# Performance work log

Measured on AMD Instinct MI355X. Metric: run time of the kernel, lower is better.

## Reference

```python
import jax, jax.numpy as jnp
import numpy as np

B, N, L = 16, 128, 512            # batch, scan length, per-step feature (= configs.seq_len)
D, S, K, R, H = 1024, 16, 4, 64, 2048  # d_model, d_state, ker_size, dt_rank, hidden_dimention


def _mamba_params(key, scale=0.02):
    ks = jax.random.split(key, 6)
    return dict(
        in_w=jax.random.normal(ks[0], (2 * D, L)) * scale,
        conv_w=jax.random.normal(ks[1], (D, K)) * scale,
        conv_b=jnp.zeros((D,)),
        xproj_w=jax.random.normal(ks[2], (R + 2 * S, D)) * scale,
        dt_w=jax.random.normal(ks[3], (D, R)) * scale,
        dt_b=jax.random.normal(ks[4], (D,)) * scale,
        A_log=jnp.tile(jnp.log(jnp.arange(1, S + 1, dtype=jnp.float32)), (D, 1)),
        Dp=jnp.ones((D,)),
        out_w=jax.random.normal(ks[5], (L, D)) * scale,
    )


def setup_inputs():
    key = jax.random.key(0)
    kx, kf, kr, k1, k2 = jax.random.split(key, 5)
    inp = {"x": jax.random.normal(kx, (B, N, L), dtype=jnp.float32)}
    for pre, k in (("f_", kf), ("r_", kr)):
        for n, v in _mamba_params(k).items():
            inp[pre + n] = v
    inp["pu_w"] = jax.random.normal(k1, (H, L)) * 0.02
    inp["pu_b"] = jnp.zeros((H,))
    inp["pl_w"] = jax.random.normal(k2, (L, H)) * 0.02
    inp["pl_b"] = jnp.zeros((L,))
    inp["ln_g"] = jnp.ones((L,))
    inp["ln_b"] = jnp.zeros((L,))
    return inp


def _ln(x, g, b, eps=1e-5):
    m = x.mean(-1, keepdims=True)
    v = ((x - m) ** 2).mean(-1, keepdims=True)
    return (x - m) * jax.lax.rsqrt(v + eps) * g + b


def _dw_causal_conv(x, w, b):
    # x: [B,N,D]; depthwise causal conv along N with kernel [D,K]
    xt = jnp.pad(x.transpose(0, 2, 1), ((0, 0), (0, 0), (K - 1, 0)))  # [B,D,N+K-1]
    y = jax.lax.conv_general_dilated(xt, w[:, None, :], (1,), 'VALID',
                                     dimension_numbers=('NCH', 'OIH', 'NCH'),
                                     feature_group_count=D)
    return (y + b[None, :, None]).transpose(0, 2, 1)


def _mamba(x, in_w, conv_w, conv_b, xproj_w, dt_w, dt_b, A_log, Dp, out_w):
    # standard Mamba block (in_proj -> depthwise conv -> silu -> selective scan -> gate -> out_proj)
    xi, res = jnp.split(x @ in_w.T, 2, axis=-1)             # [B,N,D] each
    xc = jax.nn.silu(_dw_causal_conv(xi, conv_w, conv_b))   # [B,N,D]
    dbc = xc @ xproj_w.T                                    # [B,N,R+2S]
    dt, Bm, Cm = dbc[..., :R], dbc[..., R:R + S], dbc[..., R + S:]
    delta = jax.nn.softplus(dt @ dt_w.T + dt_b)             # [B,N,D]
    A = -jnp.exp(A_log)                                     # [D,S]
    dA = jnp.exp(delta[..., None] * A)                      # [B,N,D,S]
    dBx = delta[..., None] * Bm[:, :, None, :] * xc[..., None]

    def step(h, t):
        dA_t, dBx_t, C_t = t
        h = dA_t * h + dBx_t                                # [B,D,S]
        return h, jnp.einsum('bds,bs->bd', h, C_t)

    _, ys = jax.lax.scan(step, jnp.zeros((x.shape[0], D, S), x.dtype),
                         (dA.transpose(1, 0, 2, 3), dBx.transpose(1, 0, 2, 3), Cm.transpose(1, 0, 2)))
    y = ys.transpose(1, 0, 2) + xc * Dp                     # [B,N,D]
    y = y * jax.nn.silu(res)
    return y @ out_w.T                                      # [B,N,L]


def reference(x, f_in_w, f_conv_w, f_conv_b, f_xproj_w, f_dt_w, f_dt_b, f_A_log, f_Dp, f_out_w,
              r_in_w, r_conv_w, r_conv_b, r_xproj_w, r_dt_w, r_dt_b, r_A_log, r_Dp, r_out_w,
              pu_w, pu_b, pl_w, pl_b, ln_g, ln_b):
    y1 = _mamba(x, f_in_w, f_conv_w, f_conv_b, f_xproj_w, f_dt_w, f_dt_b, f_A_log, f_Dp, f_out_w)
    y2 = _mamba(x[:, ::-1, :], r_in_w, r_conv_w, r_conv_b, r_xproj_w, r_dt_w, r_dt_b, r_A_log, r_Dp, r_out_w)
    y3 = _ln(x + y1 + y2[:, ::-1, :], ln_g, ln_b)
    yp = jax.nn.relu(y3 @ pu_w.T + pu_b)
    yp = yp @ pl_w.T + pl_b
    return _ln(yp + y3, ln_g, ln_b)
```

## Files before the change

kernel.cpp:

```cpp
#include <hip/hip_runtime.h>
#include <hip/hip_bf16.h>
#include <cstdint>

typedef __hip_bfloat16 bf16;

constexpr int Bb = 16, Nn = 128, Ll = 512, Dd = 1024, Ss = 16, Rr = 64, Hh = 2048;
constexpr int Mm = Bb * Nn;

using bf16x8 = __attribute__((ext_vector_type(8))) __bf16;
using bf16x4 = __attribute__((ext_vector_type(4))) __bf16;
using f32x4  = __attribute__((ext_vector_type(4))) float;

__device__ __forceinline__ float to_f(float x) { return x; }
__device__ __forceinline__ float to_f(bf16 x) { return __bfloat162float(x); }
__device__ __forceinline__ void store_t(float* p, float v) { *p = v; }
__device__ __forceinline__ void store_t(bf16* p, float v) { *p = __float2bfloat16(v); }
__device__ __forceinline__ __bf16 cvt1(float x) {
  bf16 h = __float2bfloat16(x);
  return *reinterpret_cast<__bf16*>(&h);
}
__device__ __forceinline__ float bfraw_to_f(__bf16 x) {
  bf16 h = *reinterpret_cast<bf16*>(&x);
  return __bfloat162float(h);
}
__device__ __forceinline__ bf16x8 load8(const bf16* p) { return *(const bf16x8*)p; }
__device__ __forceinline__ bf16x8 load8(const float* p) {
  float4 a = *(const float4*)p;
  float4 b = *(const float4*)(p + 4);
  bf16x8 r;
  r[0] = cvt1(a.x); r[1] = cvt1(a.y); r[2] = cvt1(a.z); r[3] = cvt1(a.w);
  r[4] = cvt1(b.x); r[5] = cvt1(b.y); r[6] = cvt1(b.z); r[7] = cvt1(b.w);
  return r;
}
__device__ __forceinline__ bf16x8 load8rt(const void* p, size_t idx, int isbf) {
  if (isbf) return load8((const bf16*)p + idx);
  return load8((const float*)p + idx);
}
__device__ __forceinline__ float ldf(const void* p, int i, int isbf) {
  if (isbf) return __bfloat162float(((const bf16*)p)[i]);
  return ((const float*)p)[i];
}

enum { EPI_STORE = 0, EPI_BIAS_RELU = 1, EPI_ADD = 3, EPI_BIAS = 4, EPI_BIAS_SOFTPLUS = 5,
       EPI_ATOMIC = 6 };

__global__ void sniff_kernel(const unsigned short* __restrict__ xs, int* __restrict__ flags) {
  const int tid = threadIdx.x;
  int cnt = 0;
  for (int j = 0; j < 64; ++j) {
    int i = tid + j * 256;
    unsigned short u = xs[(size_t)i * 64];
    bf16 h = *reinterpret_cast<bf16*>(&u);
    float v = __bfloat162float(h);
    float a = fabsf(v);
    if (v == 0.f || (a > 0.0009765625f && a < 16.f)) ++cnt;
  }
  __shared__ int sc[256];
  sc[tid] = cnt;
  __syncthreads();
  for (int o = 128; o > 0; o >>= 1) {
    if (tid < o) sc[tid] += sc[tid + o];
    __syncthreads();
  }
  if (tid == 0) flags[0] = (sc[0] > 8192) ? 1 : 0;
}

constexpr int LDT2 = 72;
template <typename TC, int EPI>
__global__ __launch_bounds__(256) void gemm_rt(
    const int* __restrict__ flagp,
    const void* __restrict__ A, int lda, int abf,
    const void* __restrict__ Bw, const void* __restrict__ Bw2, int ldb,
    int bmode, int bsplit,
    TC* __restrict__ C, int ldc,
    const void* __restrict__ bias, const void* __restrict__ bias2,
    int N, int Kchunk, int zk, size_t a_doff, size_t c_doff) {
  const int isbf = *flagp;
  const int ab = (abf == 2) ? isbf : abf;
  __shared__ __align__(16) __bf16 As[64 * LDT2];
  __shared__ __align__(16) __bf16 Bs[64 * LDT2];
  const int tid = threadIdx.x;
  const int wave = tid >> 6, lane = tid & 63;
  const int quad = lane >> 4, l16 = lane & 15;
  const int wm = wave & 1, wn = wave >> 1;
  int bx = blockIdx.x, by = blockIdx.y;
  const int gx = gridDim.x, gy = gridDim.y;
  if ((gx & 7) == 0) {
    int id = bx + gx * by;
    int xcd = id & 7, sl = id >> 3;
    by = sl % gy;
    bx = (sl / gy) * 8 + xcd;
  }
  int zsl = blockIdx.z;
  const void* Ap = A;
  const void* Bp0 = Bw;
  const void* biasp = bias;
  if (bmode == 3) {
    const int dir = zsl / zk;
    zsl = zsl % zk;
    if (dir) {
      Ap = (const char*)A + a_doff * (size_t)(ab ? 2 : 4);
      C += c_doff;
      Bp0 = Bw2;
      biasp = bias2;
    }
  }
  const int m0 = by * 64, n0 = bx * 64;
  const int kb = zsl * Kchunk;
  const int srow = tid >> 3;
  const int scol = (tid & 7) * 8;
  f32x4 acc[2][2] = {};
  for (int k0 = kb; k0 < kb + Kchunk; k0 += 64) {
#pragma unroll
    for (int h = 0; h < 2; ++h) {
      int r = srow + h * 32;
      *(bf16x8*)(&As[r * LDT2 + scol]) =
          load8rt(Ap, (size_t)(m0 + r) * lda + k0 + scol, ab);
      int rb = n0 + r;
      rb = rb < N ? rb : N - 1;
      const void* bp = Bp0;
      size_t bi;
      const int kk = k0 + scol;
      if (bmode == 1 && rb >= bsplit) {
        bp = Bw2; bi = (size_t)(rb - bsplit) * ldb + kk;
      } else if (bmode == 2 && kk >= bsplit) {
        bp = Bw2; bi = (size_t)rb * ldb + (kk - bsplit);
      } else {
        bi = (size_t)rb * ldb + kk;
      }
      *(bf16x8*)(&Bs[r * LDT2 + scol]) = load8rt(bp, bi, isbf);
    }
    __syncthreads();
#pragma unroll
    for (int kk2 = 0; kk2 < 2; ++kk2) {
      bf16x8 af[2], bfr[2];
#pragma unroll
      for (int i = 0; i < 2; ++i)
        af[i] = *(const bf16x8*)(&As[(wm * 32 + i * 16 + l16) * LDT2 + kk2 * 32 + quad * 8]);
#pragma unroll
      for (int j = 0; j < 2; ++j)
        bfr[j] = *(const bf16x8*)(&Bs[(wn * 32 + j * 16 + l16) * LDT2 + kk2 * 32 + quad * 8]);
#pragma unroll
      for (int i = 0; i < 2; ++i)
#pragma unroll
        for (int j = 0; j < 2; ++j)
          acc[i][j] = __builtin_amdgcn_mfma_f32_16x16x32_bf16(af[i], bfr[j], acc[i][j], 0, 0, 0);
    }
    __syncthreads();
  }
#pragma unroll
  for (int i = 0; i < 2; ++i) {
#pragma unroll
    for (int j = 0; j < 2; ++j) {
      const int col = n0 + wn * 32 + j * 16 + l16;
      if (col >= N) continue;
      float bv = 0.f;
      if (EPI == EPI_BIAS_RELU || EPI == EPI_BIAS || EPI == EPI_BIAS_SOFTPLUS)
        bv = ldf(biasp, col, isbf);
#pragma unroll
      for (int r = 0; r < 4; ++r) {
        const int row = m0 + wm * 32 + i * 16 + quad * 4 + r;
        size_t idx = (size_t)row * ldc + col;
        float v = acc[i][j][r];
        if (EPI == EPI_STORE) store_t(&C[idx], v);
        else if (EPI == EPI_BIAS_RELU) { v += bv; store_t(&C[idx], v > 0.f ? v : 0.f); }
        else if (EPI == EPI_BIAS) store_t(&C[idx], v + bv);
        else if (EPI == EPI_BIAS_SOFTPLUS) {
          v += bv;
          store_t(&C[idx], (v > 20.f) ? v : log1pf(__expf(v)));
        } else if (EPI == EPI_ATOMIC) {
          atomicAdd((float*)&C[idx], v);
        }
      }
    }
  }
}

__global__ __launch_bounds__(256) void zero_kernel(float4* __restrict__ p, int n4) {
  int i = blockIdx.x * 256 + threadIdx.x;
  if (i < n4) p[i] = float4{0.f, 0.f, 0.f, 0.f};
}

__global__ __launch_bounds__(256) void init_zbuf_rt(const int* __restrict__ flagp,
                                                    const void* __restrict__ x,
                                                    float* __restrict__ ZB) {
  const int isbf = *flagp;
  int i = blockIdx.x * 256 + threadIdx.x;
  float4 o;
  if (isbf) {
    ushort4 u = ((const ushort4*)x)[i];
    bf16 h0 = *reinterpret_cast<bf16*>(&u.x), h1 = *reinterpret_cast<bf16*>(&u.y);
    bf16 h2 = *reinterpret_cast<bf16*>(&u.z), h3 = *reinterpret_cast<bf16*>(&u.w);
    o = float4{__bfloat162float(h0), __bfloat162float(h1),
               __bfloat162float(h2), __bfloat162float(h3)};
  } else {
    o = ((const float4*)x)[i];
  }
  ((float4*)ZB)[i] = o;
}

__global__ __launch_bounds__(256) void conv_silu_rt(
    const int* __restrict__ flagp, const float* __restrict__ X2,
    const void* __restrict__ fcw, const void* __restrict__ fcb,
    const void* __restrict__ rcw, const void* __restrict__ rcb,
    float* __restrict__ XC) {
  const int isbf = *flagp;
  const int dir = blockIdx.y >> 2;
  const int d = (blockIdx.y & 3) * 256 + threadIdx.x;
  const int m = blockIdx.x;
  const int t = m & (Nn - 1);
  const void* cw = dir ? rcw : fcw;
  const void* cb = dir ? rcb : fcb;
  float w0 = ldf(cw, d * 4 + 0, isbf), w1 = ldf(cw, d * 4 + 1, isbf);
  float w2 = ldf(cw, d * 4 + 2, isbf), w3 = ldf(cw, d * 4 + 3, isbf);
  float a = ldf(cb, d, isbf);
  const size_t base = (size_t)m * 4096 + (size_t)dir * 2048 + d;
  if (dir == 0) {
    if (t >= 3) a += w0 * X2[base - 3 * 4096];
    if (t >= 2) a += w1 * X2[base - 2 * 4096];
    if (t >= 1) a += w2 * X2[base - 1 * 4096];
    a += w3 * X2[base];
  } else {
    if (t + 3 < Nn) a += w0 * X2[base + 3 * 4096];
    if (t + 2 < Nn) a += w1 * X2[base + 2 * 4096];
    if (t + 1 < Nn) a += w2 * X2[base + 1 * 4096];
    a += w3 * X2[base];
  }
  XC[(size_t)m * 2048 + (size_t)dir * 1024 + d] = a / (1.f + __expf(-a));
}

__global__ __launch_bounds__(256) void scan_gate_rt(
    const int* __restrict__ flagp,
    const float* __restrict__ DBC0, float* __restrict__ XC, const float* __restrict__ X2,
    const bf16* __restrict__ DELTA0,
    const void* __restrict__ fAlog, const void* __restrict__ fDp,
    const void* __restrict__ rAlog, const void* __restrict__ rDp) {
  const int isbf = *flagp;
  const int dir = blockIdx.z;
  const float* DBC = DBC0 + (size_t)dir * Mm * 96;
  const bf16* DELTA = DELTA0 + (size_t)dir * Mm * 1024;
  const void* A_log = dir ? rAlog : fAlog;
  const void* Dp = dir ? rDp : fDp;
  __shared__ __align__(16) __bf16 sBC[Nn * 32];
  __shared__ __align__(16) __bf16 sD[Nn * 16];
  __shared__ __align__(16) __bf16 sX[Nn * 16];
  __shared__ __align__(16) __bf16 sR[Nn * 16];
  __shared__ float sSdv[Nn * 16];
  __shared__ float sHend[4 * 16 * 16];
  __shared__ float sSdvEnd[4 * 16];
  const int b = blockIdx.x;
  const int d0 = blockIdx.y * 16;
  const int tid = threadIdx.x;
  const size_t rowbase = (size_t)b * Nn;
  const size_t xc_col = (size_t)dir * 1024;
#pragma unroll
  for (int k = 0; k < 16; ++k) {
    int idx = tid + k * 256;
    int t = idx >> 5, c = idx & 31;
    sBC[idx] = cvt1(DBC[(rowbase + t) * 96 + 64 + c]);
  }
  {
    int t = tid >> 1, h = tid & 1;
    *(uint4*)&sD[t * 16 + h * 8] = *(const uint4*)(DELTA + (rowbase + t) * 1024 + d0 + h * 8);
  }
#pragma unroll
  for (int k = 0; k < 2; ++k) {
    int j = tid + k * 256;
    int t = j >> 2, qq = j & 3;
    float4 vx = *(const float4*)(XC + (rowbase + t) * 2048 + xc_col + d0 + qq * 4);
    bf16x4 px = {cvt1(vx.x), cvt1(vx.y), cvt1(vx.z), cvt1(vx.w)};
    *(bf16x4*)&sX[t * 16 + qq * 4] = px;
    float4 vr = *(const float4*)(X2 + (rowbase + t) * 4096 + (size_t)dir * 2048 + 1024 + d0 + qq * 4);
    bf16x4 pr = {cvt1(vr.x), cvt1(vr.y), cvt1(vr.z), cvt1(vr.w)};
    *(bf16x4*)&sR[t * 16 + qq * 4] = pr;
  }
  __syncthreads();
  const int q = tid >> 6;
  const int lane = tid & 63;
  const int dl = lane & 15, sg = lane >> 4;
  const int d = d0 + dl;
  float A_[4];
#pragma unroll
  for (int j = 0; j < 4; ++j) A_[j] = -__expf(ldf(A_log, d * Ss + sg * 4 + j, isbf));
  float h0 = 0.f, h1 = 0.f, h2 = 0.f, h3 = 0.f, Sdv = 0.f;
  for (int j = 0; j < 32; ++j) {
    const int p = q * 32 + j;
    const int t = dir ? (Nn - 1 - p) : p;
    const float dv = bfraw_to_f(sD[t * 16 + dl]);
    const float xv = bfraw_to_f(sX[t * 16 + dl]);
    Sdv += dv;
    bf16x4 Bmv = *(const bf16x4*)&sBC[t * 32 + sg * 4];
    bf16x4 Cmv = *(const bf16x4*)&sBC[t * 32 + 16 + sg * 4];
    const float dx = dv * xv;
    h0 = __expf(dv * A_[0]) * h0 + dx * bfraw_to_f(Bmv[0]);
    h1 = __expf(dv * A_[1]) * h1 + dx * bfraw_to_f(Bmv[1]);
    h2 = __expf(dv * A_[2]) * h2 + dx * bfraw_to_f(Bmv[2]);
    h3 = __expf(dv * A_[3]) * h3 + dx * bfraw_to_f(Bmv[3]);
    float acc = h0 * bfraw_to_f(Cmv[0]) + h1 * bfraw_to_f(Cmv[1]) +
                h2 * bfraw_to_f(Cmv[2]) + h3 * bfraw_to_f(Cmv[3]);
    acc += __shfl_xor(acc, 16, 64);
    acc += __shfl_xor(acc, 32, 64);
    if (sg == 0) {
      sSdv[t * 16 + dl] = Sdv;
      XC[(rowbase + t) * 2048 + xc_col + d] = acc;
    }
  }
  sHend[q * 256 + (sg * 4 + 0) * 16 + dl] = h0;
  sHend[q * 256 + (sg * 4 + 1) * 16 + dl] = h1;
  sHend[q * 256 + (sg * 4 + 2) * 16 + dl] = h2;
  sHend[q * 256 + (sg * 4 + 3) * 16 + dl] = h3;
  if (sg == 0) sSdvEnd[q * 16 + dl] = Sdv;
  __syncthreads();
  if (q == 0) {
    float r0 = 0.f, r1 = 0.f, r2 = 0.f, r3 = 0.f;
    for (int qq = 0; qq < 4; ++qq) {
      const float se = sSdvEnd[qq * 16 + dl];
      const float e0 = __expf(A_[0] * se), e1 = __expf(A_[1] * se);
      const float e2 = __expf(A_[2] * se), e3 = __expf(A_[3] * se);
      const int base = qq * 256 + sg * 4 * 16 + dl;
      float t0 = sHend[base + 0 * 16], t1 = sHend[base + 1 * 16];
      float t2 = sHend[base + 2 * 16], t3 = sHend[base + 3 * 16];
      sHend[base + 0 * 16] = r0; sHend[base + 1 * 16] = r1;
      sHend[base + 2 * 16] = r2; sHend[base + 3 * 16] = r3;
      r0 = e0 * r0 + t0; r1 = e1 * r1 + t1;
      r2 = e2 * r2 + t2; r3 = e3 * r3 + t3;
    }
  }
  __syncthreads();
  {
    const int dl2 = lane & 15, trow = lane >> 4;
    const int d2 = d0 + dl2;
    float A2[16];
#pragma unroll
    for (int s = 0; s < 16; ++s) A2[s] = -__expf(ldf(A_log, d2 * Ss + s, isbf));
    const float dp2 = ldf(Dp, d2, isbf);
    float hin[16];
#pragma unroll
    for (int s = 0; s < 16; ++s) hin[s] = sHend[q * 256 + s * 16 + dl2];
    for (int rep = 0; rep < 8; ++rep) {
      const int p = q * 32 + trow + rep * 4;
      const int t = dir ? (Nn - 1 - p) : p;
      const float Sv = sSdv[t * 16 + dl2];
      float corr = 0.f;
#pragma unroll
      for (int s = 0; s < 16; ++s)
        corr += bfraw_to_f(sBC[t * 32 + 16 + s]) * __expf(A2[s] * Sv) * hin[s];
      const size_t gidx = (rowbase + t) * 2048 + xc_col + d2;
      const float y = XC[gidx] + corr;
      const float xv = bfraw_to_f(sX[t * 16 + dl2]);
      const float res = bfraw_to_f(sR[t * 16 + dl2]);
      const float g = res / (1.f + __expf(-res));
      XC[gidx] = (y + xv * dp2) * g;
    }
  }
}

template <int MODE>
__global__ __launch_bounds__(256) void ln_rt(const int* __restrict__ flagp,
                                             const float* __restrict__ Z,
                                             const float* __restrict__ Zadd,
                                             const void* __restrict__ g,
                                             const void* __restrict__ bb,
                                             const void* __restrict__ pb,
                                             void* __restrict__ outp) {
  const int isbf = *flagp;
  const int row = blockIdx.x;
  const int tid = threadIdx.x;
  const int c0 = tid * 2;
  const float2* z = (const float2*)(Z + (size_t)row * Ll);
  float2 v = z[tid];
  if (MODE == 1) {
    const float2* za = (const float2*)(Zadd + (size_t)row * Ll);
    float2 a = za[tid];
    v.x += a.x + ldf(pb, c0, isbf);
    v.y += a.y + ldf(pb, c0 + 1, isbf);
  }
  float s = v.x + v.y, q = v.x * v.x + v.y * v.y;
#pragma unroll
  for (int o = 32; o > 0; o >>= 1) {
    s += __shfl_xor(s, o, 64);
    q += __shfl_xor(q, o, 64);
  }
  __shared__ float ss[4], qq[4];
  const int wv = tid >> 6, ln = tid & 63;
  if (ln == 0) { ss[wv] = s; qq[wv] = q; }
  __syncthreads();
  s = ss[0] + ss[1] + ss[2] + ss[3];
  q = qq[0] + qq[1] + qq[2] + qq[3];
  const float mean = s * (1.f / Ll);
  const float var = q * (1.f / Ll) - mean * mean;
  const float rs = rsqrtf(var + 1e-5f);
  const float o0 = (v.x - mean) * rs * ldf(g, c0, isbf) + ldf(bb, c0, isbf);
  const float o1 = (v.y - mean) * rs * ldf(g, c0 + 1, isbf) + ldf(bb, c0 + 1, isbf);
  if (MODE == 0) {
    float* out = (float*)outp;
    out[(size_t)row * Ll + c0] = o0;
    out[(size_t)row * Ll + c0 + 1] = o1;
  } else {
    if (isbf) {
      bf16* out = (bf16*)outp;
      out[(size_t)row * Ll + c0] = __float2bfloat16(o0);
      out[(size_t)row * Ll + c0 + 1] = __float2bfloat16(o1);
    } else {
      float* out = (float*)outp;
      out[(size_t)row * Ll + c0] = o0;
      out[(size_t)row * Ll + c0 + 1] = o1;
    }
  }
}

extern "C" void kernel_launch(void* const* d_in, const int* in_sizes, int n_in, void* d_out,
                              int out_size, void* d_ws, size_t ws_size, hipStream_t stream) {
  char* ws = (char*)d_ws;
  int* flags = (int*)ws;
  float* X2 = (float*)(ws + 256);
  float* XC = X2 + (size_t)Mm * 4096;
  float* DBC = XC + (size_t)Mm * 2048;
  float* Z2 = DBC + (size_t)2 * Mm * 96;
  float* ZB = Z2 + (size_t)Mm * 512;
  float* Y3 = ZB + (size_t)Mm * 512;
  bf16* DELTA = (bf16*)(Y3 + (size_t)Mm * 512);
  bf16* H1 = (bf16*)X2;
  size_t needed = 256 + sizeof(float) * ((size_t)Mm * 4096 + (size_t)Mm * 2048 +
                                         (size_t)2 * Mm * 96 + (size_t)3 * Mm * 512 +
                                         (size_t)Mm * 1024);
  if (ws_size < needed) return;

  const void* x = d_in[0];
  const dim3 blk(256);

  sniff_kernel<<<dim3(1), blk, 0, stream>>>((const unsigned short*)x, flags);
  init_zbuf_rt<<<dim3(Mm * Ll / 4 / 256), blk, 0, stream>>>(flags, x, ZB);
  zero_kernel<<<dim3((2 * Mm * 96 + Mm * 512) / 4 / 256), blk, 0, stream>>>(
      (float4*)DBC, (2 * Mm * 96 + Mm * 512) / 4);
  gemm_rt<float, EPI_STORE><<<dim3(64, 32), blk, 0, stream>>>(
      flags, x, Ll, 2, d_in[1], d_in[10], Ll, 1, 2048,
      X2, 4096, nullptr, nullptr, 4096, Ll, 1, 0, 0);
  conv_silu_rt<<<dim3(Mm, 8), blk, 0, stream>>>(flags, X2, d_in[2], d_in[3],
                                                d_in[11], d_in[12], XC);
  gemm_rt<float, EPI_ATOMIC><<<dim3(2, 32, 8), blk, 0, stream>>>(
      flags, XC, 2048, 0, d_in[4], d_in[13], Dd, 3, 0,
      DBC, 96, nullptr, nullptr, 96, 256, 4, 1024, (size_t)Mm * 96);
  gemm_rt<bf16, EPI_BIAS_SOFTPLUS><<<dim3(16, 32, 2), blk, 0, stream>>>(
      flags, DBC, 96, 0, d_in[5], d_in[14], Rr, 3, 0,
      DELTA, 1024, d_in[6], d_in[15], 1024, Rr, 1, (size_t)Mm * 96, (size_t)Mm * 1024);
  scan_gate_rt<<<dim3(Bb, Dd / 16, 2), blk, 0, stream>>>(
      flags, DBC, XC, X2, DELTA, d_in[7], d_in[8], d_in[16], d_in[17]);
  gemm_rt<float, EPI_ATOMIC><<<dim3(8, 32, 4), blk, 0, stream>>>(
      flags, XC, 2048, 0, d_in[9], d_in[18], Dd, 2, 1024,
      ZB, Ll, nullptr, nullptr, Ll, 512, 1, 0, 0);
  ln_rt<0><<<dim3(Mm), blk, 0, stream>>>(flags, ZB, nullptr, d_in[23], d_in[24], nullptr, (void*)Y3);
  gemm_rt<bf16, EPI_BIAS_RELU><<<dim3(32, 32), blk, 0, stream>>>(
      flags, Y3, Ll, 0, d_in[19], nullptr, Ll, 0, 0,
      H1, Hh, d_in[20], nullptr, Hh, Ll, 1, 0, 0);
  gemm_rt<float, EPI_ATOMIC><<<dim3(8, 32, 2), blk, 0, stream>>>(
      flags, H1, Hh, 1, d_in[21], nullptr, Hh, 0, 0,
      Z2, Ll, nullptr, nullptr, Ll, 1024, 1, 0, 0);
  ln_rt<1><<<dim3(Mm), blk, 0, stream>>>(flags, Z2, Y3, d_in[23], d_in[24], d_in[22], d_out);

  (void)in_sizes; (void)n_in; (void)out_size;
}
```

Baseline: 373.4 us.

## Add 128x128-tile GEMM for large projections and recompute scan outputs in second pass

Adds a gemm128 kernel with 128x128 output tiles, 4x4 MFMA fragments per wave and XCD-aware block remapping, and uses it for the in_proj, out_proj and both MLP GEMMs to raise operand reuse per LDS load. The selective-scan kernel no longer writes partial outputs and cumulative delta sums in its first chunk pass. Instead it reruns each chunk's recurrence from the exchanged carry-in states, producing outputs directly and dropping the 16-term exp correction pass and the sSdv buffer. The small-GEMM kernel loses its split-B addressing path. Larger tiles mean fewer blocks and more register pressure, and the scan now does the recurrence twice per chunk.

```diff
diff --git a/kernel.cpp b/kernel.cpp
--- a/kernel.cpp
+++ b/kernel.cpp
@@ -66,6 +66,7 @@
 }
 
 constexpr int LDT2 = 72;
+
 template <typename TC, int EPI>
 __global__ __launch_bounds__(256) void gemm_rt(
     const int* __restrict__ flagp,
@@ -118,17 +119,8 @@
           load8rt(Ap, (size_t)(m0 + r) * lda + k0 + scol, ab);
       int rb = n0 + r;
       rb = rb < N ? rb : N - 1;
-      const void* bp = Bp0;
-      size_t bi;
-      const int kk = k0 + scol;
-      if (bmode == 1 && rb >= bsplit) {
-        bp = Bw2; bi = (size_t)(rb - bsplit) * ldb + kk;
-      } else if (bmode == 2 && kk >= bsplit) {
-        bp = Bw2; bi = (size_t)rb * ldb + (kk - bsplit);
-      } else {
-        bi = (size_t)rb * ldb + kk;
-      }
-      *(bf16x8*)(&Bs[r * LDT2 + scol]) = load8rt(bp, bi, isbf);
+      size_t bi = (size_t)rb * ldb + k0 + scol;
+      *(bf16x8*)(&Bs[r * LDT2 + scol]) = load8rt(Bp0, bi, isbf);
     }
     __syncthreads();
 #pragma unroll
@@ -171,6 +163,93 @@
         } else if (EPI == EPI_ATOMIC) {
           atomicAdd((float*)&C[idx], v);
         }
+      }
+    }
+  }
+}
+
+template <typename TC, int EPI>
+__global__ __launch_bounds__(256) void gemm128(
+    const int* __restrict__ flagp,
+    const void* __restrict__ A, int lda, int abf,
+    const void* __restrict__ Bw, const void* __restrict__ Bw2, int ldb,
+    int bmode, int bsplit,
+    TC* __restrict__ C, int ldc,
+    const void* __restrict__ bias,
+    int N, int Kchunk) {
+  const int isbf = *flagp;
+  const int ab = (abf == 2) ? isbf : abf;
+  __shared__ __align__(16) __bf16 As[128 * LDT2];
+  __shared__ __align__(16) __bf16 Bs[128 * LDT2];
+  const int tid = threadIdx.x;
+  const int wave = tid >> 6, lane = tid & 63;
+  const int quad = lane >> 4, l16 = lane & 15;
+  const int wm = wave & 1, wn = wave >> 1;
+  int bx = blockIdx.x, by = blockIdx.y;
+  const int gx = gridDim.x, gy = gridDim.y;
+  if ((gx & 7) == 0) {
+    int id = bx + gx * by;
+    int xcd = id & 7, sl = id >> 3;
+    by = sl % gy;
+    bx = (sl / gy) * 8 + xcd;
+  }
+  const int m0 = by * 128, n0 = bx * 128;
+  const int kb = blockIdx.z * Kchunk;
+  const int srow = tid >> 3;
+  const int scol = (tid & 7) * 8;
+  f32x4 acc[4][4] = {};
+  for (int k0 = kb; k0 < kb + Kchunk; k0 += 64) {
+#pragma unroll
+    for (int h = 0; h < 4; ++h) {
+      int r = srow + h * 32;
+      *(bf16x8*)(&As[r * LDT2 + scol]) =
+          load8rt(A, (size_t)(m0 + r) * lda + k0 + scol, ab);
+      const int rb = n0 + r;
+      const int kk = k0 + scol;
+      const void* bp = Bw;
+      size_t bi;
+      if (bmode == 1 && rb >= bsplit) {
+        bp = Bw2; bi = (size_t)(rb - bsplit) * ldb + kk;
+      } else if (bmode == 2 && kk >= bsplit) {
+        bp = Bw2; bi = (size_t)rb * ldb + (kk - bsplit);
+      } else {
+        bi = (size_t)rb * ldb + kk;
+      }
+      *(bf16x8*)(&Bs[r * LDT2 + scol]) = load8rt(bp, bi, isbf);
+    }
+    __syncthreads();
+#pragma unroll
+    for (int kk2 = 0; kk2 < 2; ++kk2) {
+      bf16x8 af[4], bfr[4];
+#pragma unroll
+      for (int i = 0; i < 4; ++i)
+        af[i] = *(const bf16x8*)(&As[(wm * 64 + i * 16 + l16) * LDT2 + kk2 * 32 + quad * 8]);
+#pragma unroll
+      for (int j = 0; j < 4; ++j)
+        bfr[j] = *(const bf16x8*)(&Bs[(wn * 64 + j * 16 + l16) * LDT2 + kk2 * 32 + quad * 8]);
+#pragma unroll
+      for (int i = 0; i < 4; ++i)
+#pragma unroll
+        for (int j = 0; j < 4; ++j)
+          acc[i][j] = __builtin_amdgcn_mfma_f32_16x16x32_bf16(af[i], bfr[j], acc[i][j], 0, 0, 0);
+    }
+    __syncthreads();
+  }
+#pragma unroll
+  for (int i = 0; i < 4; ++i) {
+#pragma unroll
+    for (int j = 0; j < 4; ++j) {
+      const int col = n0 + wn * 64 + j * 16 + l16;
+      float bv = 0.f;
+      if (EPI == EPI_BIAS_RELU) bv = ldf(bias, col, isbf);
+#pragma unroll
+      for (int r = 0; r < 4; ++r) {
+        const int row = m0 + wm * 64 + i * 16 + quad * 4 + r;
+        size_t idx = (size_t)row * ldc + col;
+        float v = acc[i][j][r];
+        if (EPI == EPI_STORE) store_t(&C[idx], v);
+        else if (EPI == EPI_BIAS_RELU) { v += bv; store_t(&C[idx], v > 0.f ? v : 0.f); }
+        else if (EPI == EPI_ATOMIC) atomicAdd((float*)&C[idx], v);
       }
     }
   }
@@ -229,7 +308,7 @@
   XC[(size_t)m * 2048 + (size_t)dir * 1024 + d] = a / (1.f + __expf(-a));
 }
 
-__global__ __launch_bounds__(256) void scan_gate_rt(
+__global__ __launch_bounds__(256) void scan_gate2(
     const int* __restrict__ flagp,
     const float* __restrict__ DBC0, float* __restrict__ XC, const float* __restrict__ X2,
     const bf16* __restrict__ DELTA0,
@@ -245,7 +324,6 @@
   __shared__ __align__(16) __bf16 sD[Nn * 16];
   __shared__ __align__(16) __bf16 sX[Nn * 16];
   __shared__ __align__(16) __bf16 sR[Nn * 16];
-  __shared__ float sSdv[Nn * 16];
   __shared__ float sHend[4 * 16 * 16];
   __shared__ float sSdvEnd[4 * 16];
   const int b = blockIdx.x;
@@ -290,20 +368,11 @@
     const float xv = bfraw_to_f(sX[t * 16 + dl]);
     Sdv += dv;
     bf16x4 Bmv = *(const bf16x4*)&sBC[t * 32 + sg * 4];
-    bf16x4 Cmv = *(const bf16x4*)&sBC[t * 32 + 16 + sg * 4];
     const float dx = dv * xv;
     h0 = __expf(dv * A_[0]) * h0 + dx * bfraw_to_f(Bmv[0]);
     h1 = __expf(dv * A_[1]) * h1 + dx * bfraw_to_f(Bmv[1]);
     h2 = __expf(dv * A_[2]) * h2 + dx * bfraw_to_f(Bmv[2]);
     h3 = __expf(dv * A_[3]) * h3 + dx * bfraw_to_f(Bmv[3]);
-    float acc = h0 * bfraw_to_f(Cmv[0]) + h1 * bfraw_to_f(Cmv[1]) +
-                h2 * bfraw_to_f(Cmv[2]) + h3 * bfraw_to_f(Cmv[3]);
-    acc += __shfl_xor(acc, 16, 64);
-    acc += __shfl_xor(acc, 32, 64);
-    if (sg == 0) {
-      sSdv[t * 16 + dl] = Sdv;
-      XC[(rowbase + t) * 2048 + xc_col + d] = acc;
-    }
   }
   sHend[q * 256 + (sg * 4 + 0) * 16 + dl] = h0;
   sHend[q * 256 + (sg * 4 + 1) * 16 + dl] = h1;
@@ -327,30 +396,31 @@
     }
   }
   __syncthreads();
-  {
-    const int dl2 = lane & 15, trow = lane >> 4;
-    const int d2 = d0 + dl2;
-    float A2[16];
-#pragma unroll
-    for (int s = 0; s < 16; ++s) A2[s] = -__expf(ldf(A_log, d2 * Ss + s, isbf));
-    const float dp2 = ldf(Dp, d2, isbf);
-    float hin[16];
-#pragma unroll
-    for (int s = 0; s < 16; ++s) hin[s] = sHend[q * 256 + s * 16 + dl2];
-    for (int rep = 0; rep < 8; ++rep) {
-      const int p = q * 32 + trow + rep * 4;
-      const int t = dir ? (Nn - 1 - p) : p;
-      const float Sv = sSdv[t * 16 + dl2];
-      float corr = 0.f;
-#pragma unroll
-      for (int s = 0; s < 16; ++s)
-        corr += bfraw_to_f(sBC[t * 32 + 16 + s]) * __expf(A2[s] * Sv) * hin[s];
-      const size_t gidx = (rowbase + t) * 2048 + xc_col + d2;
-      const float y = XC[gidx] + corr;
-      const float xv = bfraw_to_f(sX[t * 16 + dl2]);
-      const float res = bfraw_to_f(sR[t * 16 + dl2]);
+  h0 = sHend[q * 256 + (sg * 4 + 0) * 16 + dl];
+  h1 = sHend[q * 256 + (sg * 4 + 1) * 16 + dl];
+  h2 = sHend[q * 256 + (sg * 4 + 2) * 16 + dl];
+  h3 = sHend[q * 256 + (sg * 4 + 3) * 16 + dl];
+  const float dp = ldf(Dp, d, isbf);
+  for (int j = 0; j < 32; ++j) {
+    const int p = q * 32 + j;
+    const int t = dir ? (Nn - 1 - p) : p;
+    const float dv = bfraw_to_f(sD[t * 16 + dl]);
+    const float xv = bfraw_to_f(sX[t * 16 + dl]);
+    bf16x4 Bmv = *(const bf16x4*)&sBC[t * 32 + sg * 4];
+    bf16x4 Cmv = *(const bf16x4*)&sBC[t * 32 + 16 + sg * 4];
+    const float dx = dv * xv;
+    h0 = __expf(dv * A_[0]) * h0 + dx * bfraw_to_f(Bmv[0]);
+    h1 = __expf(dv * A_[1]) * h1 + dx * bfraw_to_f(Bmv[1]);
+    h2 = __expf(dv * A_[2]) * h2 + dx * bfraw_to_f(Bmv[2]);
+    h3 = __expf(dv * A_[3]) * h3 + dx * bfraw_to_f(Bmv[3]);
+    float acc = h0 * bfraw_to_f(Cmv[0]) + h1 * bfraw_to_f(Cmv[1]) +
+                h2 * bfraw_to_f(Cmv[2]) + h3 * bfraw_to_f(Cmv[3]);
+    acc += __shfl_xor(acc, 16, 64);
+    acc += __shfl_xor(acc, 32, 64);
+    if (sg == 0) {
+      const float res = bfraw_to_f(sR[t * 16 + dl]);
       const float g = res / (1.f + __expf(-res));
-      XC[gidx] = (y + xv * dp2) * g;
+      XC[(rowbase + t) * 2048 + xc_col + d] = (acc + xv * dp) * g;
     }
   }
 }
@@ -433,9 +503,9 @@
   init_zbuf_rt<<<dim3(Mm * Ll / 4 / 256), blk, 0, stream>>>(flags, x, ZB);
   zero_kernel<<<dim3((2 * Mm * 96 + Mm * 512) / 4 / 256), blk, 0, stream>>>(
       (float4*)DBC, (2 * Mm * 96 + Mm * 512) / 4);
-  gemm_rt<float, EPI_STORE><<<dim3(64, 32), blk, 0, stream>>>(
+  gemm128<float, EPI_STORE><<<dim3(32, 16), blk, 0, stream>>>(
       flags, x, Ll, 2, d_in[1], d_in[10], Ll, 1, 2048,
-      X2, 4096, nullptr, nullptr, 4096, Ll, 1, 0, 0);
+      X2, 4096, nullptr, 4096, Ll);
   conv_silu_rt<<<dim3(Mm, 8), blk, 0, stream>>>(flags, X2, d_in[2], d_in[3],
                                                 d_in[11], d_in[12], XC);
   gemm_rt<float, EPI_ATOMIC><<<dim3(2, 32, 8), blk, 0, stream>>>(
@@ -444,18 +514,18 @@
   gemm_rt<bf16, EPI_BIAS_SOFTPLUS><<<dim3(16, 32, 2), blk, 0, stream>>>(
       flags, DBC, 96, 0, d_in[5], d_in[14], Rr, 3, 0,
       DELTA, 1024, d_in[6], d_in[15], 1024, Rr, 1, (size_t)Mm * 96, (size_t)Mm * 1024);
-  scan_gate_rt<<<dim3(Bb, Dd / 16, 2), blk, 0, stream>>>(
+  scan_gate2<<<dim3(Bb, Dd / 16, 2), blk, 0, stream>>>(
       flags, DBC, XC, X2, DELTA, d_in[7], d_in[8], d_in[16], d_in[17]);
-  gemm_rt<float, EPI_ATOMIC><<<dim3(8, 32, 4), blk, 0, stream>>>(
+  gemm128<float, EPI_ATOMIC><<<dim3(4, 16, 4), blk, 0, stream>>>(
       flags, XC, 2048, 0, d_in[9], d_in[18], Dd, 2, 1024,
-      ZB, Ll, nullptr, nullptr, Ll, 512, 1, 0, 0);
+      ZB, Ll, nullptr, Ll, 512);
   ln_rt<0><<<dim3(Mm), blk, 0, stream>>>(flags, ZB, nullptr, d_in[23], d_in[24], nullptr, (void*)Y3);
-  gemm_rt<bf16, EPI_BIAS_RELU><<<dim3(32, 32), blk, 0, stream>>>(
+  gemm128<bf16, EPI_BIAS_RELU><<<dim3(16, 16), blk, 0, stream>>>(
       flags, Y3, Ll, 0, d_in[19], nullptr, Ll, 0, 0,
-      H1, Hh, d_in[20], nullptr, Hh, Ll, 1, 0, 0);
-  gemm_rt<float, EPI_ATOMIC><<<dim3(8, 32, 2), blk, 0, stream>>>(
+      H1, Hh, d_in[20], Hh, Ll);
+  gemm128<float, EPI_ATOMIC><<<dim3(4, 16, 4), blk, 0, stream>>>(
       flags, H1, Hh, 1, d_in[21], nullptr, Hh, 0, 0,
-      Z2, Ll, nullptr, nullptr, Ll, 1024, 1, 0, 0);
+      Z2, Ll, nullptr, Ll, 512);
   ln_rt<1><<<dim3(Mm), blk, 0, stream>>>(flags, Z2, Y3, d_in[23], d_in[24], d_in[22], d_out);
 
   (void)in_sizes; (void)n_in; (void)out_size;
```

Result: slower. 414.8 us (+11.1%).

## Store Mamba intermediates in bf16 and recompute chunked scan instead of correction pass

Applied to the files above, without the earlier changes.

The in-projection output and the conv/silu activations move from fp32 to bf16 buffers, roughly halving traffic for the conv, x-projection, scan and out-projection stages. The scan kernel no longer writes partial outputs and then fixes them with a 16-term exponential correction. It now runs a first pass to get chunk-end states, combines them, and reruns the recurrence from the correct starting state, caching delta and x in registers. This removes global read-modify-write and shared prefix-sum storage at the cost of doing the recurrence twice, higher register pressure, and bf16 rounding of the intermediates.

```diff
diff --git a/kernel.cpp b/kernel.cpp
--- a/kernel.cpp
+++ b/kernel.cpp
@@ -66,6 +66,7 @@
 }
 
 constexpr int LDT2 = 72;
+
 template <typename TC, int EPI>
 __global__ __launch_bounds__(256) void gemm_rt(
     const int* __restrict__ flagp,
@@ -200,10 +201,10 @@
 }
 
 __global__ __launch_bounds__(256) void conv_silu_rt(
-    const int* __restrict__ flagp, const float* __restrict__ X2,
+    const int* __restrict__ flagp, const bf16* __restrict__ X2b,
     const void* __restrict__ fcw, const void* __restrict__ fcb,
     const void* __restrict__ rcw, const void* __restrict__ rcb,
-    float* __restrict__ XC) {
+    bf16* __restrict__ XCb) {
   const int isbf = *flagp;
   const int dir = blockIdx.y >> 2;
   const int d = (blockIdx.y & 3) * 256 + threadIdx.x;
@@ -216,22 +217,23 @@
   float a = ldf(cb, d, isbf);
   const size_t base = (size_t)m * 4096 + (size_t)dir * 2048 + d;
   if (dir == 0) {
-    if (t >= 3) a += w0 * X2[base - 3 * 4096];
-    if (t >= 2) a += w1 * X2[base - 2 * 4096];
-    if (t >= 1) a += w2 * X2[base - 1 * 4096];
-    a += w3 * X2[base];
+    if (t >= 3) a += w0 * to_f(X2b[base - 3 * 4096]);
+    if (t >= 2) a += w1 * to_f(X2b[base - 2 * 4096]);
+    if (t >= 1) a += w2 * to_f(X2b[base - 1 * 4096]);
+    a += w3 * to_f(X2b[base]);
   } else {
-    if (t + 3 < Nn) a += w0 * X2[base + 3 * 4096];
-    if (t + 2 < Nn) a += w1 * X2[base + 2 * 4096];
-    if (t + 1 < Nn) a += w2 * X2[base + 1 * 4096];
-    a += w3 * X2[base];
-  }
-  XC[(size_t)m * 2048 + (size_t)dir * 1024 + d] = a / (1.f + __expf(-a));
-}
-
-__global__ __launch_bounds__(256) void scan_gate_rt(
+    if (t + 3 < Nn) a += w0 * to_f(X2b[base + 3 * 4096]);
+    if (t + 2 < Nn) a += w1 * to_f(X2b[base + 2 * 4096]);
+    if (t + 1 < Nn) a += w2 * to_f(X2b[base + 1 * 4096]);
+    a += w3 * to_f(X2b[base]);
+  }
+  const float s = a / (1.f + __expf(-a));
+  XCb[(size_t)m * 2048 + (size_t)dir * 1024 + d] = __float2bfloat16(s);
+}
+
+__global__ __launch_bounds__(256) void scan_gate2(
     const int* __restrict__ flagp,
-    const float* __restrict__ DBC0, float* __restrict__ XC, const float* __restrict__ X2,
+    const float* __restrict__ DBC0, bf16* __restrict__ XCb, const bf16* __restrict__ X2b,
     const bf16* __restrict__ DELTA0,
     const void* __restrict__ fAlog, const void* __restrict__ fDp,
     const void* __restrict__ rAlog, const void* __restrict__ rDp) {
@@ -245,7 +247,6 @@
   __shared__ __align__(16) __bf16 sD[Nn * 16];
   __shared__ __align__(16) __bf16 sX[Nn * 16];
   __shared__ __align__(16) __bf16 sR[Nn * 16];
-  __shared__ float sSdv[Nn * 16];
   __shared__ float sHend[4 * 16 * 16];
   __shared__ float sSdvEnd[4 * 16];
   const int b = blockIdx.x;
@@ -262,17 +263,10 @@
   {
     int t = tid >> 1, h = tid & 1;
     *(uint4*)&sD[t * 16 + h * 8] = *(const uint4*)(DELTA + (rowbase + t) * 1024 + d0 + h * 8);
-  }
-#pragma unroll
-  for (int k = 0; k < 2; ++k) {
-    int j = tid + k * 256;
-    int t = j >> 2, qq = j & 3;
-    float4 vx = *(const float4*)(XC + (rowbase + t) * 2048 + xc_col + d0 + qq * 4);
-    bf16x4 px = {cvt1(vx.x), cvt1(vx.y), cvt1(vx.z), cvt1(vx.w)};
-    *(bf16x4*)&sX[t * 16 + qq * 4] = px;
-    float4 vr = *(const float4*)(X2 + (rowbase + t) * 4096 + (size_t)dir * 2048 + 1024 + d0 + qq * 4);
-    bf16x4 pr = {cvt1(vr.x), cvt1(vr.y), cvt1(vr.z), cvt1(vr.w)};
-    *(bf16x4*)&sR[t * 16 + qq * 4] = pr;
+    *(uint4*)&sX[t * 16 + h * 8] =
+        *(const uint4*)(XCb + (rowbase + t) * 2048 + xc_col + d0 + h * 8);
+    *(uint4*)&sR[t * 16 + h * 8] =
+        *(const uint4*)(X2b + (rowbase + t) * 4096 + (size_t)dir * 2048 + 1024 + d0 + h * 8);
   }
   __syncthreads();
   const int q = tid >> 6;
@@ -282,28 +276,23 @@
   float A_[4];
 #pragma unroll
   for (int j = 0; j < 4; ++j) A_[j] = -__expf(ldf(A_log, d * Ss + sg * 4 + j, isbf));
+  float dvr[32], xvr[32];
   float h0 = 0.f, h1 = 0.f, h2 = 0.f, h3 = 0.f, Sdv = 0.f;
+#pragma unroll
   for (int j = 0; j < 32; ++j) {
     const int p = q * 32 + j;
     const int t = dir ? (Nn - 1 - p) : p;
     const float dv = bfraw_to_f(sD[t * 16 + dl]);
     const float xv = bfraw_to_f(sX[t * 16 + dl]);
+    dvr[j] = dv;
+    xvr[j] = xv;
     Sdv += dv;
     bf16x4 Bmv = *(const bf16x4*)&sBC[t * 32 + sg * 4];
-    bf16x4 Cmv = *(const bf16x4*)&sBC[t * 32 + 16 + sg * 4];
     const float dx = dv * xv;
     h0 = __expf(dv * A_[0]) * h0 + dx * bfraw_to_f(Bmv[0]);
     h1 = __expf(dv * A_[1]) * h1 + dx * bfraw_to_f(Bmv[1]);
     h2 = __expf(dv * A_[2]) * h2 + dx * bfraw_to_f(Bmv[2]);
     h3 = __expf(dv * A_[3]) * h3 + dx * bfraw_to_f(Bmv[3]);
-    float acc = h0 * bfraw_to_f(Cmv[0]) + h1 * bfraw_to_f(Cmv[1]) +
-                h2 * bfraw_to_f(Cmv[2]) + h3 * bfraw_to_f(Cmv[3]);
-    acc += __shfl_xor(acc, 16, 64);
-    acc += __shfl_xor(acc, 32, 64);
-    if (sg == 0) {
-      sSdv[t * 16 + dl] = Sdv;
-      XC[(rowbase + t) * 2048 + xc_col + d] = acc;
-    }
   }
   sHend[q * 256 + (sg * 4 + 0) * 16 + dl] = h0;
   sHend[q * 256 + (sg * 4 + 1) * 16 + dl] = h1;
@@ -327,30 +316,32 @@
     }
   }
   __syncthreads();
-  {
-    const int dl2 = lane & 15, trow = lane >> 4;
-    const int d2 = d0 + dl2;
-    float A2[16];
-#pragma unroll
-    for (int s = 0; s < 16; ++s) A2[s] = -__expf(ldf(A_log, d2 * Ss + s, isbf));
-    const float dp2 = ldf(Dp, d2, isbf);
-    float hin[16];
-#pragma unroll
-    for (int s = 0; s < 16; ++s) hin[s] = sHend[q * 256 + s * 16 + dl2];
-    for (int rep = 0; rep < 8; ++rep) {
-      const int p = q * 32 + trow + rep * 4;
-      const int t = dir ? (Nn - 1 - p) : p;
-      const float Sv = sSdv[t * 16 + dl2];
-      float corr = 0.f;
-#pragma unroll
-      for (int s = 0; s < 16; ++s)
-        corr += bfraw_to_f(sBC[t * 32 + 16 + s]) * __expf(A2[s] * Sv) * hin[s];
-      const size_t gidx = (rowbase + t) * 2048 + xc_col + d2;
-      const float y = XC[gidx] + corr;
-      const float xv = bfraw_to_f(sX[t * 16 + dl2]);
-      const float res = bfraw_to_f(sR[t * 16 + dl2]);
+  h0 = sHend[q * 256 + (sg * 4 + 0) * 16 + dl];
+  h1 = sHend[q * 256 + (sg * 4 + 1) * 16 + dl];
+  h2 = sHend[q * 256 + (sg * 4 + 2) * 16 + dl];
+  h3 = sHend[q * 256 + (sg * 4 + 3) * 16 + dl];
+  const float dp = ldf(Dp, d, isbf);
+#pragma unroll
+  for (int j = 0; j < 32; ++j) {
+    const int p = q * 32 + j;
+    const int t = dir ? (Nn - 1 - p) : p;
+    const float dv = dvr[j];
+    const float xv = xvr[j];
+    bf16x4 Bmv = *(const bf16x4*)&sBC[t * 32 + sg * 4];
+    bf16x4 Cmv = *(const bf16x4*)&sBC[t * 32 + 16 + sg * 4];
+    const float dx = dv * xv;
+    h0 = __expf(dv * A_[0]) * h0 + dx * bfraw_to_f(Bmv[0]);
+    h1 = __expf(dv * A_[1]) * h1 + dx * bfraw_to_f(Bmv[1]);
+    h2 = __expf(dv * A_[2]) * h2 + dx * bfraw_to_f(Bmv[2]);
+    h3 = __expf(dv * A_[3]) * h3 + dx * bfraw_to_f(Bmv[3]);
+    float acc = h0 * bfraw_to_f(Cmv[0]) + h1 * bfraw_to_f(Cmv[1]) +
+                h2 * bfraw_to_f(Cmv[2]) + h3 * bfraw_to_f(Cmv[3]);
+    acc += __shfl_xor(acc, 16, 64);
+    acc += __shfl_xor(acc, 32, 64);
+    if (sg == 0) {
+      const float res = bfraw_to_f(sR[t * 16 + dl]);
       const float g = res / (1.f + __expf(-res));
-      XC[gidx] = (y + xv * dp2) * g;
+      XCb[(rowbase + t) * 2048 + xc_col + d] = __float2bfloat16((acc + xv * dp) * g);
     }
   }
 }
@@ -413,17 +404,16 @@
                               int out_size, void* d_ws, size_t ws_size, hipStream_t stream) {
   char* ws = (char*)d_ws;
   int* flags = (int*)ws;
-  float* X2 = (float*)(ws + 256);
-  float* XC = X2 + (size_t)Mm * 4096;
-  float* DBC = XC + (size_t)Mm * 2048;
+  bf16* X2b = (bf16*)(ws + 256);
+  bf16* XCb = X2b + (size_t)Mm * 4096;
+  float* DBC = (float*)(XCb + (size_t)Mm * 2048);
   float* Z2 = DBC + (size_t)2 * Mm * 96;
   float* ZB = Z2 + (size_t)Mm * 512;
   float* Y3 = ZB + (size_t)Mm * 512;
   bf16* DELTA = (bf16*)(Y3 + (size_t)Mm * 512);
-  bf16* H1 = (bf16*)X2;
-  size_t needed = 256 + sizeof(float) * ((size_t)Mm * 4096 + (size_t)Mm * 2048 +
-                                         (size_t)2 * Mm * 96 + (size_t)3 * Mm * 512 +
-                                         (size_t)Mm * 1024);
+  bf16* H1 = X2b;
+  size_t needed = 256 + 2 * ((size_t)Mm * 4096 + (size_t)Mm * 2048 + (size_t)2 * Mm * 1024) +
+                  4 * ((size_t)2 * Mm * 96 + (size_t)3 * Mm * 512);
   if (ws_size < needed) return;
 
   const void* x = d_in[0];
@@ -433,21 +423,21 @@
   init_zbuf_rt<<<dim3(Mm * Ll / 4 / 256), blk, 0, stream>>>(flags, x, ZB);
   zero_kernel<<<dim3((2 * Mm * 96 + Mm * 512) / 4 / 256), blk, 0, stream>>>(
       (float4*)DBC, (2 * Mm * 96 + Mm * 512) / 4);
-  gemm_rt<float, EPI_STORE><<<dim3(64, 32), blk, 0, stream>>>(
+  gemm_rt<bf16, EPI_STORE><<<dim3(64, 32), blk, 0, stream>>>(
       flags, x, Ll, 2, d_in[1], d_in[10], Ll, 1, 2048,
-      X2, 4096, nullptr, nullptr, 4096, Ll, 1, 0, 0);
-  conv_silu_rt<<<dim3(Mm, 8), blk, 0, stream>>>(flags, X2, d_in[2], d_in[3],
-                                                d_in[11], d_in[12], XC);
+      X2b, 4096, nullptr, nullptr, 4096, Ll, 1, 0, 0);
+  conv_silu_rt<<<dim3(Mm, 8), blk, 0, stream>>>(flags, X2b, d_in[2], d_in[3],
+                                                d_in[11], d_in[12], XCb);
   gemm_rt<float, EPI_ATOMIC><<<dim3(2, 32, 8), blk, 0, stream>>>(
-      flags, XC, 2048, 0, d_in[4], d_in[13], Dd, 3, 0,
+      flags, XCb, 2048, 1, d_in[4], d_in[13], Dd, 3, 0,
       DBC, 96, nullptr, nullptr, 96, 256, 4, 1024, (size_t)Mm * 96);
   gemm_rt<bf16, EPI_BIAS_SOFTPLUS><<<dim3(16, 32, 2), blk, 0, stream>>>(
       flags, DBC, 96, 0, d_in[5], d_in[14], Rr, 3, 0,
       DELTA, 1024, d_in[6], d_in[15], 1024, Rr, 1, (size_t)Mm * 96, (size_t)Mm * 1024);
-  scan_gate_rt<<<dim3(Bb, Dd / 16, 2), blk, 0, stream>>>(
-      flags, DBC, XC, X2, DELTA, d_in[7], d_in[8], d_in[16], d_in[17]);
+  scan_gate2<<<dim3(Bb, Dd / 16, 2), blk, 0, stream>>>(
+      flags, DBC, XCb, X2b, DELTA, d_in[7], d_in[8], d_in[16], d_in[17]);
   gemm_rt<float, EPI_ATOMIC><<<dim3(8, 32, 4), blk, 0, stream>>>(
-      flags, XC, 2048, 0, d_in[9], d_in[18], Dd, 2, 1024,
+      flags, XCb, 2048, 1, d_in[9], d_in[18], Dd, 2, 1024,
       ZB, Ll, nullptr, nullptr, Ll, 512, 1, 0, 0);
   ln_rt<0><<<dim3(Mm), blk, 0, stream>>>(flags, ZB, nullptr, d_in[23], d_in[24], nullptr, (void*)Y3);
   gemm_rt<bf16, EPI_BIAS_RELU><<<dim3(32, 32), blk, 0, stream>>>(
```

New measurement: 423.0 us. 13.3% more time.
